# Kernel optimization log

Hardware: AMD Instinct MI355X
Metric: run time of the kernel (lower is better)

The kernel has to match this reference:

```python
import jax, jax.numpy as jnp
import numpy as np

EMBED = 1024
HEADS = 16
HEAD_DIM = EMBED // HEADS


def setup_inputs() -> dict:
    key = jax.random.key(0)
    ks = jax.random.split(key, 11)
    B, S = 4, 2048
    scale = 0.02
    inp = {
        "value": jax.random.normal(ks[0], (B, S, EMBED), jnp.float32),
        "key": jax.random.normal(ks[1], (B, S, EMBED), jnp.float32),
        "query": jax.random.normal(ks[2], (B, S, EMBED), jnp.float32),
        "Wv": jax.random.normal(ks[3], (EMBED, EMBED), jnp.float32) * scale,
        "bv": jax.random.normal(ks[4], (EMBED,), jnp.float32) * scale,
        "Wk": jax.random.normal(ks[5], (EMBED, EMBED), jnp.float32) * scale,
        "bk": jax.random.normal(ks[6], (EMBED,), jnp.float32) * scale,
        "Wq": jax.random.normal(ks[7], (EMBED, EMBED), jnp.float32) * scale,
        "bq": jax.random.normal(ks[8], (EMBED,), jnp.float32) * scale,
        "Wo": jax.random.normal(ks[9], (EMBED, EMBED), jnp.float32) * scale,
        "bo": jax.random.normal(ks[10], (EMBED,), jnp.float32) * scale,
    }
    return inp


def reference(value, key, query, Wv, bv, Wk, bk, Wq, bq, Wo, bo):
    B, Sq, E = query.shape
    # linear projections (torch Linear: x @ W.T + b; here W stored as [in, out])
    v = (value @ Wv + bv).reshape(B, -1, HEADS, HEAD_DIM)   # [B,Skv,H,D]
    k = (key @ Wk + bk).reshape(B, -1, HEADS, HEAD_DIM)
    q = (query @ Wq + bq).reshape(B, Sq, HEADS, HEAD_DIM)
    # scaled dot-product attention, full score matrix [B,H,Sq,Skv]
    energy = jnp.einsum("bqhd,bkhd->bhqk", q, k) / jnp.sqrt(jnp.float32(HEAD_DIM))
    attn = jax.nn.softmax(energy, axis=-1)
    out = jnp.einsum("bhqk,bkhd->bqhd", attn, v).reshape(B, Sq, E)
    return out @ Wo + bo
```

## Files before the change

### kernel.cpp

```cpp
#include <hip/hip_runtime.h>
#include <hip/hip_bf16.h>
#include <stdint.h>

typedef unsigned short u16;
typedef __bf16 bf16_t;
typedef bf16_t bf16x8 __attribute__((ext_vector_type(8)));
typedef float f32x4 __attribute__((ext_vector_type(4)));

__device__ __forceinline__ u16 f2b(float f) {
    union { float f; uint32_t i; } v; v.f = f;
    uint32_t r = v.i + 0x7FFFu + ((v.i >> 16) & 1u);
    return (u16)(r >> 16);
}
__device__ __forceinline__ uint32_t pk2(float a, float b) {
    __hip_bfloat162 h = __float22bfloat162_rn(float2{a, b});
    return *(const uint32_t*)&h;
}
__device__ __forceinline__ uint4 pack8(float4 lo, float4 hi) {
    uint4 r;
    r.x = pk2(lo.x, lo.y); r.y = pk2(lo.z, lo.w);
    r.z = pk2(hi.x, hi.y); r.w = pk2(hi.z, hi.w);
    return r;
}
__device__ __forceinline__ void async16(const u16* g, u16* l) {
    __builtin_amdgcn_global_load_lds(
        (const __attribute__((address_space(1))) uint32_t*)g,
        (__attribute__((address_space(3))) uint32_t*)l,
        16, 0, 0);
}

template<bool XF32>
__device__ __forceinline__ void gemm128(const void* __restrict__ Xv,
                                        const u16* __restrict__ WT,
                                        const float* __restrict__ bias,
                                        u16* __restrict__ dstb,
                                        float* __restrict__ dstf, int mode)
{
    __shared__ __align__(16) u16 As[128 * 64];
    __shared__ __align__(16) u16 Bs[128 * 64];
    const int t    = threadIdx.x;
    const int lane = t & 63;
    const int quad = lane >> 4;
    const int l15  = lane & 15;
    const int m0 = blockIdx.y * 128;
    const int n0 = blockIdx.x * 128;
    const int wave = t >> 6;
    const int wm = (wave >> 1) * 64;
    const int wn = (wave & 1) * 64;

    f32x4 acc[4][4];
#pragma unroll
    for (int i = 0; i < 4; i++)
#pragma unroll
        for (int j = 0; j < 4; j++)
#pragma unroll
            for (int r = 0; r < 4; r++) acc[i][j][r] = 0.0f;

    int rr[4], lb[4];
#pragma unroll
    for (int c = 0; c < 4; c++) {
        const int ci = c * 256 + t;
        rr[c] = ci >> 3;
        lb[c] = (ci & 7) ^ (rr[c] & 7);
    }

    for (int kt = 0; kt < 1024; kt += 64) {
        __syncthreads();
#pragma unroll
        for (int c = 0; c < 4; c++)
            async16(WT + (n0 + rr[c]) * 1024 + kt + lb[c] * 8, &Bs[(c * 256 + t) * 8]);
        if (XF32) {
#pragma unroll
            for (int c = 0; c < 4; c++) {
                const float* g = (const float*)Xv + (m0 + rr[c]) * 1024 + kt + lb[c] * 8;
                const float4 lo = *(const float4*)g;
                const float4 hi = *(const float4*)(g + 4);
                *(uint4*)&As[(c * 256 + t) * 8] = pack8(lo, hi);
            }
        } else {
#pragma unroll
            for (int c = 0; c < 4; c++)
                async16((const u16*)Xv + (m0 + rr[c]) * 1024 + kt + lb[c] * 8,
                        &As[(c * 256 + t) * 8]);
        }
        __syncthreads();

#pragma unroll
        for (int kk = 0; kk < 64; kk += 32) {
            bf16x8 af[4], bfv[4];
#pragma unroll
            for (int i = 0; i < 4; i++) {
                const int ra = wm + i * 16 + l15;
                const int rb2 = wn + i * 16 + l15;
                af[i]  = *(const bf16x8*)&As[ra * 64 + (((kk >> 3) + quad) ^ (l15 & 7)) * 8];
                bfv[i] = *(const bf16x8*)&Bs[rb2 * 64 + (((kk >> 3) + quad) ^ (l15 & 7)) * 8];
            }
#pragma unroll
            for (int i = 0; i < 4; i++)
#pragma unroll
                for (int j = 0; j < 4; j++)
                    acc[i][j] = __builtin_amdgcn_mfma_f32_16x16x32_bf16(af[i], bfv[j], acc[i][j], 0, 0, 0);
        }
    }

#pragma unroll
    for (int i = 0; i < 4; i++) {
        const int rb = m0 + wm + i * 16 + quad * 4;
#pragma unroll
        for (int j = 0; j < 4; j++) {
            const int col = n0 + wn + j * 16 + l15;
            const float bias_v = bias[col];
            if (mode == 2) {
                const int b = rb >> 11, s = rb & 2047;
                const int h = col >> 6, d = col & 63;
                uint2 pk;
                pk.x = pk2(acc[i][j][0] + bias_v, acc[i][j][1] + bias_v);
                pk.y = pk2(acc[i][j][2] + bias_v, acc[i][j][3] + bias_v);
                *(uint2*)&dstb[((b * 16 + h) * 64 + d) * 2048 + s] = pk;
            } else {
#pragma unroll
                for (int r = 0; r < 4; r++) {
                    const float v = acc[i][j][r] + bias_v;
                    const int gm = rb + r;
                    if (mode == 0) {
                        const int b = gm >> 11, s = gm & 2047;
                        const int h = col >> 6, d = col & 63;
                        dstb[((b * 16 + h) * 2048 + s) * 64 + d] = f2b(v);
                    } else {
                        dstf[gm * 1024 + col] = v;
                    }
                }
            }
        }
    }
}

__global__ __launch_bounds__(256)
void convert_x(const float* __restrict__ q_in, const float* __restrict__ k_in,
               const float* __restrict__ v_in, u16* __restrict__ Xb)
{
    const int z = blockIdx.y;
    const float* src = (z == 0) ? q_in : (z == 1) ? k_in : v_in;
    u16* dst = Xb + z * (8 * 1024 * 1024);
    const int i = (blockIdx.x * 256 + threadIdx.x) * 8;
    const float4 lo = *(const float4*)(src + i);
    const float4 hi = *(const float4*)(src + i + 4);
    *(uint4*)(dst + i) = pack8(lo, hi);
}

__global__ __launch_bounds__(256)
void qkv_kernel_f32(const float* __restrict__ q_in, const float* __restrict__ k_in,
                    const float* __restrict__ v_in, const u16* __restrict__ WT,
                    const float* __restrict__ bq, const float* __restrict__ bk,
                    const float* __restrict__ bv,
                    u16* __restrict__ Qo, u16* __restrict__ Ko, u16* __restrict__ VTo)
{
    const int z = blockIdx.z;
    const float* X   = (z == 0) ? q_in : (z == 1) ? k_in : v_in;
    const u16* wt    = WT + ((z == 0) ? 2 : (z == 1) ? 1 : 0) * (1024 * 1024);
    const float* bias= (z == 0) ? bq : (z == 1) ? bk : bv;
    u16* dst         = (z == 0) ? Qo : (z == 1) ? Ko : VTo;
    gemm128<true>(X, wt, bias, dst, nullptr, (z == 2) ? 2 : 0);
}

__global__ __launch_bounds__(256)
void qkv_kernel_b16(const u16* __restrict__ Xb, const u16* __restrict__ WT,
                    const float* __restrict__ bq, const float* __restrict__ bk,
                    const float* __restrict__ bv,
                    u16* __restrict__ Qo, u16* __restrict__ Ko, u16* __restrict__ VTo)
{
    const int z = blockIdx.z;
    const u16* X     = Xb + z * (8 * 1024 * 1024);
    const u16* wt    = WT + ((z == 0) ? 2 : (z == 1) ? 1 : 0) * (1024 * 1024);
    const float* bias= (z == 0) ? bq : (z == 1) ? bk : bv;
    u16* dst         = (z == 0) ? Qo : (z == 1) ? Ko : VTo;
    gemm128<false>(X, wt, bias, dst, nullptr, (z == 2) ? 2 : 0);
}

__global__ __launch_bounds__(256)
void oproj_kernel(const u16* __restrict__ AO, const u16* __restrict__ WT,
                  const float* __restrict__ bo, float* __restrict__ out)
{
    gemm128<false>(AO, WT + 3 * 1024 * 1024, bo, nullptr, out, 1);
}

__global__ void transpose_w(const float* __restrict__ Wv, const float* __restrict__ Wk,
                            const float* __restrict__ Wq, const float* __restrict__ Wo,
                            u16* __restrict__ WT)
{
    __shared__ u16 tile[64][65];
    const int z = blockIdx.z;
    const float* W = (z == 0) ? Wv : (z == 1) ? Wk : (z == 2) ? Wq : Wo;
    u16* dst = WT + z * 1024 * 1024;
    const int r0 = blockIdx.y * 64, c0 = blockIdx.x * 64;
    const int col = threadIdx.x & 63, rb = threadIdx.x >> 6;
#pragma unroll
    for (int r = rb; r < 64; r += 4) tile[r][col] = f2b(W[(r0 + r) * 1024 + c0 + col]);
    __syncthreads();
#pragma unroll
    for (int r = rb; r < 64; r += 4) dst[(c0 + r) * 1024 + r0 + col] = tile[col][r];
}

__global__ __launch_bounds__(256, 3)
void attn_kernel(const u16* __restrict__ Q, const u16* __restrict__ K,
                 const u16* __restrict__ VT, u16* __restrict__ AO)
{
    __shared__ __align__(16) u16 KPs[128 * 64];
    __shared__ __align__(16) u16 Vts[64 * 128];

    const int t    = threadIdx.x;
    const int lane = t & 63;
    const int wave = t >> 6;
    const int quad = lane >> 4;
    const int l15  = lane & 15;
    const int bh = blockIdx.y;
    const int qt = blockIdx.x;

    const u16* Qg = Q + (bh * 2048 + qt * 64) * 64;
    const u16* Kg = K + bh * 2048 * 64;
    const u16* Vg = VT + bh * 64 * 2048;

    bf16x8 bqr[2];
    {
        const u16* qrow = Qg + (wave * 16 + l15) * 64 + quad * 8;
#pragma unroll
        for (int c = 0; c < 2; c++) {
            uint4 dv = *(const uint4*)(qrow + c * 32);
            u16 tmp[8];
            *(uint4*)tmp = dv;
            float f[8];
#pragma unroll
            for (int i = 0; i < 8; i++) {
                union { float f; uint32_t u; } x; x.u = ((uint32_t)tmp[i]) << 16;
                f[i] = x.f * 0.18033688f;
            }
            uint4 pk;
            pk.x = pk2(f[0], f[1]); pk.y = pk2(f[2], f[3]);
            pk.z = pk2(f[4], f[5]); pk.w = pk2(f[6], f[7]);
            bqr[c] = *(bf16x8*)&pk;
        }
    }

    f32x4 o[4];
#pragma unroll
    for (int dj = 0; dj < 4; dj++)
#pragma unroll
        for (int r = 0; r < 4; r++) o[dj][r] = 0.0f;
    float m_st = -1.0e30f, l_st = 0.0f;

    const u16* kgp[4];
    const u16* vgp[4];
    u16* kld[4];
    u16* vld[4];
#pragma unroll
    for (int c = 0; c < 4; c++) {
        const int ci = c * 256 + t;
        const int krr = ci >> 3, klb = (ci & 7)  ^ (krr & 7);
        const int vrr = ci >> 4, vlb = (ci & 15) ^ (vrr & 15);
        kgp[c] = Kg + krr * 64 + klb * 8;
        vgp[c] = Vg + vrr * 2048 + vlb * 8;
        kld[c] = &KPs[ci * 8];
        vld[c] = &Vts[ci * 8];
    }
    int ak_off[2][8];
#pragma unroll
    for (int ki = 0; ki < 2; ki++)
#pragma unroll
        for (int n = 0; n < 8; n++)
            ak_off[ki][n] = (n * 16 + l15) * 64 + (((ki * 4) + quad) ^ (l15 & 7)) * 8;
    int av_off[4][4], bp_off[4], pw_off[8];
#pragma unroll
    for (int ks = 0; ks < 4; ks++) {
        bp_off[ks] = (wave * 16 + l15) * 128 + ((ks * 4 + quad) ^ l15) * 8;
#pragma unroll
        for (int dj = 0; dj < 4; dj++)
            av_off[ks][dj] = (dj * 16 + l15) * 128 + ((ks * 4 + quad) ^ l15) * 8;
    }
#pragma unroll
    for (int n = 0; n < 8; n++)
        pw_off[n] = (wave * 16 + l15) * 128 + ((2 * n + (quad >> 1)) ^ l15) * 8
                    + (quad & 1) * 4;

    for (int kv = 0; kv < 16; kv++) {
        __syncthreads();
#pragma unroll
        for (int c = 0; c < 4; c++) {
            async16(kgp[c], kld[c]);
            async16(vgp[c], vld[c]);
        }
        __syncthreads();

        f32x4 s[8];
#pragma unroll
        for (int n = 0; n < 8; n++)
#pragma unroll
            for (int r = 0; r < 4; r++) s[n][r] = 0.0f;
#pragma unroll
        for (int ki = 0; ki < 2; ki++) {
            const bf16x8 bq = bqr[ki];
#pragma unroll
            for (int n = 0; n < 8; n++) {
                const bf16x8 ak = *(const bf16x8*)&KPs[ak_off[ki][n]];
                s[n] = __builtin_amdgcn_mfma_f32_16x16x32_bf16(ak, bq, s[n], 0, 0, 0);
            }
        }
        __syncthreads();

        float mxn[8];
#pragma unroll
        for (int n = 0; n < 8; n++)
            mxn[n] = fmaxf(fmaxf(s[n][0], s[n][1]), fmaxf(s[n][2], s[n][3]));
        float mx = fmaxf(fmaxf(fmaxf(mxn[0], mxn[1]), fmaxf(mxn[2], mxn[3])),
                         fmaxf(fmaxf(mxn[4], mxn[5]), fmaxf(mxn[6], mxn[7])));
        mx = fmaxf(mx, __shfl_xor(mx, 16));
        mx = fmaxf(mx, __shfl_xor(mx, 32));
        const float mnew = fmaxf(m_st, mx);
        const float alpha = exp2f(m_st - mnew);
        m_st = mnew;
        float sum = 0.0f;
#pragma unroll
        for (int n = 0; n < 8; n++)
#pragma unroll
            for (int r = 0; r < 4; r++) {
                const float p = exp2f(s[n][r] - m_st);
                s[n][r] = p;
                sum += p;
            }
        sum += __shfl_xor(sum, 16);
        sum += __shfl_xor(sum, 32);
        l_st = l_st * alpha + sum;
#pragma unroll
        for (int dj = 0; dj < 4; dj++)
#pragma unroll
            for (int r = 0; r < 4; r++) o[dj][r] *= alpha;

#pragma unroll
        for (int n = 0; n < 8; n++) {
            uint2 pk;
            pk.x = pk2(s[n][0], s[n][1]);
            pk.y = pk2(s[n][2], s[n][3]);
            *(uint2*)&KPs[pw_off[n]] = pk;
        }
        asm volatile("s_waitcnt lgkmcnt(0)" ::: "memory");

#pragma unroll
        for (int ks = 0; ks < 4; ks++) {
            const bf16x8 bp = *(const bf16x8*)&KPs[bp_off[ks]];
#pragma unroll
            for (int dj = 0; dj < 4; dj++) {
                const bf16x8 av = *(const bf16x8*)&Vts[av_off[ks][dj]];
                o[dj] = __builtin_amdgcn_mfma_f32_16x16x32_bf16(av, bp, o[dj], 0, 0, 0);
            }
        }

#pragma unroll
        for (int c = 0; c < 4; c++) {
            kgp[c] += 128 * 64;
            vgp[c] += 128;
        }
    }

    const int b = bh >> 4, h = bh & 15;
    const int sq = qt * 64 + wave * 16 + l15;
    const float inv = 1.0f / l_st;
#pragma unroll
    for (int dj = 0; dj < 4; dj++) {
        uint2 pk;
        pk.x = pk2(o[dj][0] * inv, o[dj][1] * inv);
        pk.y = pk2(o[dj][2] * inv, o[dj][3] * inv);
        *(uint2*)&AO[(b * 2048 + sq) * 1024 + h * 64 + dj * 16 + quad * 4] = pk;
    }
}

extern "C" void kernel_launch(void* const* d_in, const int* in_sizes, int n_in,
                              void* d_out, int out_size, void* d_ws, size_t ws_size,
                              hipStream_t stream)
{
    (void)in_sizes; (void)n_in; (void)out_size;
    const float* value = (const float*)d_in[0];
    const float* key_  = (const float*)d_in[1];
    const float* query = (const float*)d_in[2];
    const float* Wv = (const float*)d_in[3];
    const float* bv = (const float*)d_in[4];
    const float* Wk = (const float*)d_in[5];
    const float* bk = (const float*)d_in[6];
    const float* Wq = (const float*)d_in[7];
    const float* bq = (const float*)d_in[8];
    const float* Wo = (const float*)d_in[9];
    const float* bo = (const float*)d_in[10];

    u16* ws = (u16*)d_ws;
    u16* WT = ws;
    u16* Q  = ws + 4 * 1024 * 1024;
    u16* K  = Q + 8 * 1024 * 1024;
    u16* VT = K + 8 * 1024 * 1024;
    u16* AO = VT + 8 * 1024 * 1024;
    u16* Xb = AO + 8 * 1024 * 1024;
    const size_t need = (size_t)(4 + 8 + 8 + 8 + 8 + 24) * 1024 * 1024 * sizeof(u16);

    transpose_w<<<dim3(16, 16, 4), dim3(256), 0, stream>>>(Wv, Wk, Wq, Wo, WT);
    if (ws_size >= need) {
        convert_x<<<dim3(4096, 3), dim3(256), 0, stream>>>(query, key_, value, Xb);
        qkv_kernel_b16<<<dim3(8, 64, 3), dim3(256), 0, stream>>>(Xb, WT, bq, bk, bv,
                                                                 Q, K, VT);
    } else {
        qkv_kernel_f32<<<dim3(8, 64, 3), dim3(256), 0, stream>>>(query, key_, value,
                                                                 WT, bq, bk, bv,
                                                                 Q, K, VT);
    }
    attn_kernel<<<dim3(32, 64), dim3(256), 0, stream>>>(Q, K, VT, AO);
    oproj_kernel<<<dim3(8, 64, 1), dim3(256), 0, stream>>>(AO, WT, bo, (float*)d_out);
}
```

Measured before the change: 415.3 us.

## Compute softmax denominator via ones-row MFMA and use lazy max rescaling

Appends a ones row (plus zero padding) to the V tile in shared memory so that an extra MFMA accumulates the row sum of P. This removes the scalar sum and shuffle reductions. The running max is now only updated when some lane's tile max exceeds the current reference by more than 8 (log2 units), which skips most rescales of the accumulators. The max is folded into the MFMA accumulator initialisation. The cost is 25% more MFMAs in the PV step, extra LDS, and a denominator built from bf16-rounded P values.

```diff
diff --git a/kernel.cpp b/kernel.cpp
--- a/kernel.cpp
+++ b/kernel.cpp
@@ -206,7 +206,7 @@
                  const u16* __restrict__ VT, u16* __restrict__ AO)
 {
     __shared__ __align__(16) u16 KPs[128 * 64];
-    __shared__ __align__(16) u16 Vts[64 * 128];
+    __shared__ __align__(16) u16 Vts[80 * 128];
 
     const int t    = threadIdx.x;
     const int lane = t & 63;
@@ -220,6 +220,16 @@
     const u16* Kg = K + bh * 2048 * 64;
     const u16* Vg = VT + bh * 64 * 2048;
 
+    {
+        const int idx = t * 8;
+        const int row = 64 + (idx >> 7);
+        const u16 one = 0x3F80;
+        u16 vals[8];
+#pragma unroll
+        for (int i = 0; i < 8; i++) vals[i] = (row == 64) ? one : (u16)0;
+        *(uint4*)&Vts[64 * 128 + idx] = *(uint4*)vals;
+    }
+
     bf16x8 bqr[2];
     {
         const u16* qrow = Qg + (wave * 16 + l15) * 64 + quad * 8;
@@ -241,12 +251,12 @@
         }
     }
 
-    f32x4 o[4];
-#pragma unroll
-    for (int dj = 0; dj < 4; dj++)
+    f32x4 o[5];
+#pragma unroll
+    for (int dj = 0; dj < 5; dj++)
 #pragma unroll
         for (int r = 0; r < 4; r++) o[dj][r] = 0.0f;
-    float m_st = -1.0e30f, l_st = 0.0f;
+    float m_st = 0.0f;
 
     const u16* kgp[4];
     const u16* vgp[4];
@@ -268,12 +278,12 @@
 #pragma unroll
         for (int n = 0; n < 8; n++)
             ak_off[ki][n] = (n * 16 + l15) * 64 + (((ki * 4) + quad) ^ (l15 & 7)) * 8;
-    int av_off[4][4], bp_off[4], pw_off[8];
+    int av_off[4][5], bp_off[4], pw_off[8];
 #pragma unroll
     for (int ks = 0; ks < 4; ks++) {
         bp_off[ks] = (wave * 16 + l15) * 128 + ((ks * 4 + quad) ^ l15) * 8;
 #pragma unroll
-        for (int dj = 0; dj < 4; dj++)
+        for (int dj = 0; dj < 5; dj++)
             av_off[ks][dj] = (dj * 16 + l15) * 128 + ((ks * 4 + quad) ^ l15) * 8;
     }
 #pragma unroll
@@ -294,7 +304,7 @@
 #pragma unroll
         for (int n = 0; n < 8; n++)
 #pragma unroll
-            for (int r = 0; r < 4; r++) s[n][r] = 0.0f;
+            for (int r = 0; r < 4; r++) s[n][r] = -m_st;
 #pragma unroll
         for (int ki = 0; ki < 2; ki++) {
             const bf16x8 bq = bqr[ki];
@@ -314,31 +324,25 @@
                          fmaxf(fmaxf(mxn[4], mxn[5]), fmaxf(mxn[6], mxn[7])));
         mx = fmaxf(mx, __shfl_xor(mx, 16));
         mx = fmaxf(mx, __shfl_xor(mx, 32));
-        const float mnew = fmaxf(m_st, mx);
-        const float alpha = exp2f(m_st - mnew);
-        m_st = mnew;
-        float sum = 0.0f;
-#pragma unroll
-        for (int n = 0; n < 8; n++)
-#pragma unroll
-            for (int r = 0; r < 4; r++) {
-                const float p = exp2f(s[n][r] - m_st);
-                s[n][r] = p;
-                sum += p;
-            }
-        sum += __shfl_xor(sum, 16);
-        sum += __shfl_xor(sum, 32);
-        l_st = l_st * alpha + sum;
-#pragma unroll
-        for (int dj = 0; dj < 4; dj++)
-#pragma unroll
-            for (int r = 0; r < 4; r++) o[dj][r] *= alpha;
+        if (__any(mx > 8.0f)) {
+            const float dm = fmaxf(mx, 0.0f);
+            const float alpha = exp2f(-dm);
+#pragma unroll
+            for (int n = 0; n < 8; n++)
+#pragma unroll
+                for (int r = 0; r < 4; r++) s[n][r] -= dm;
+            m_st += dm;
+#pragma unroll
+            for (int dj = 0; dj < 5; dj++)
+#pragma unroll
+                for (int r = 0; r < 4; r++) o[dj][r] *= alpha;
+        }
 
 #pragma unroll
         for (int n = 0; n < 8; n++) {
             uint2 pk;
-            pk.x = pk2(s[n][0], s[n][1]);
-            pk.y = pk2(s[n][2], s[n][3]);
+            pk.x = pk2(exp2f(s[n][0]), exp2f(s[n][1]));
+            pk.y = pk2(exp2f(s[n][2]), exp2f(s[n][3]));
             *(uint2*)&KPs[pw_off[n]] = pk;
         }
         asm volatile("s_waitcnt lgkmcnt(0)" ::: "memory");
@@ -347,7 +351,7 @@
         for (int ks = 0; ks < 4; ks++) {
             const bf16x8 bp = *(const bf16x8*)&KPs[bp_off[ks]];
 #pragma unroll
-            for (int dj = 0; dj < 4; dj++) {
+            for (int dj = 0; dj < 5; dj++) {
                 const bf16x8 av = *(const bf16x8*)&Vts[av_off[ks][dj]];
                 o[dj] = __builtin_amdgcn_mfma_f32_16x16x32_bf16(av, bp, o[dj], 0, 0, 0);
             }
@@ -360,9 +364,10 @@
         }
     }
 
+    const float lsum = __shfl(o[4][0], l15);
     const int b = bh >> 4, h = bh & 15;
     const int sq = qt * 64 + wave * 16 + l15;
-    const float inv = 1.0f / l_st;
+    const float inv = 1.0f / lsum;
 #pragma unroll
     for (int dj = 0; dj < 4; dj++) {
         uint2 pk;
```

Result: faster. 391.7 us (-5.7%).
